# Performance work log

Hardware: AMD Instinct MI355X
Metric: run time of the kernel (lower is better)

Reference implementation:

```python
import jax, jax.numpy as jnp
import numpy as np

TWO_PI = 2.0 * np.pi
DAMP_VERTICAL = 1.0
DAMP_HORIZONTAL = 0.0


def _var(p, q, ra, rb, wvno, xka, xkb, dpth):
    # surf96 'var': layer eigenfunction products with evanescent-scaling (exp(-pex-sex))
    ra_s = jnp.where(ra > 0, ra, 1.0)
    rb_s = jnp.where(rb > 0, rb, 1.0)
    # P branch
    sinp_o = jnp.sin(p)
    fac_p = jnp.where(p < 16.0, jnp.exp(-2.0 * p), 0.0)
    cosp_e = (1.0 + fac_p) * 0.5
    sinp_e = (1.0 - fac_p) * 0.5
    lt_a = wvno < xka
    gt_a = wvno > xka
    pex = jnp.where(gt_a, p, 0.0)
    cosp = jnp.where(lt_a, jnp.cos(p), jnp.where(gt_a, cosp_e, 1.0))
    w = jnp.where(lt_a, sinp_o / ra_s, jnp.where(gt_a, sinp_e / ra_s, dpth))
    x = jnp.where(lt_a, -ra * sinp_o, jnp.where(gt_a, ra * sinp_e, 0.0))
    # S branch
    sinq_o = jnp.sin(q)
    fac_q = jnp.where(q < 16.0, jnp.exp(-2.0 * q), 0.0)
    cosq_e = (1.0 + fac_q) * 0.5
    sinq_e = (1.0 - fac_q) * 0.5
    lt_b = wvno < xkb
    gt_b = wvno > xkb
    sex = jnp.where(gt_b, q, 0.0)
    cosq = jnp.where(lt_b, jnp.cos(q), jnp.where(gt_b, cosq_e, 1.0))
    y = jnp.where(lt_b, sinq_o / rb_s, jnp.where(gt_b, sinq_e / rb_s, dpth))
    z = jnp.where(lt_b, -rb * sinq_o, jnp.where(gt_b, rb * sinq_e, 0.0))
    exa = pex + sex
    a0 = jnp.where(exa < 60.0, jnp.exp(-exa), 0.0)
    return (a0, cosp * cosq, cosp * y, cosp * z, cosq * w, cosq * x,
            x * y, x * z, w * y, w * z)


def _dnka(wvno2, gam, gammk, rho, a0, cpcq, cpy, cpz, cqw, cqx, xy, xz, wy, wz):
    # Dunkin's 5x5 compound matrix
    gamm1 = gam - 1.0
    twgm1 = gam + gamm1
    gmgmk = gam * gammk
    gmgm1 = gam * gamm1
    gm1sq = gamm1 * gamm1
    rho2 = rho * rho
    a0pq = a0 - cpcq
    t = -2.0 * wvno2
    c00 = cpcq - 2.0 * gmgm1 * a0pq - gmgmk * xz - wvno2 * gm1sq * wy
    c01 = (wvno2 * cpy - cqx) / rho
    c02 = -(twgm1 * a0pq + gammk * xz + wvno2 * gamm1 * wy) / rho
    c03 = (cpz - wvno2 * cqw) / rho
    c04 = -(2.0 * wvno2 * a0pq + xz + wvno2 * wvno2 * wy) / rho2
    c10 = (gmgmk * cpz - gm1sq * cqw) * rho
    c11 = cpcq
    c12 = gammk * cpz - gamm1 * cqw
    c13 = -wz
    c30 = (gm1sq * cpy - gmgmk * cqx) * rho
    c31 = -xy
    c32 = gamm1 * cpy - gammk * cqx
    c40 = -(2.0 * gmgmk * gm1sq * a0pq + gmgmk * gmgmk * xz + gm1sq * gm1sq * wy) * rho2
    c42 = -(gammk * gamm1 * twgm1 * a0pq + gam * gammk * gammk * xz + gamm1 * gm1sq * wy) * rho
    c20 = t * c42
    c21 = t * c32
    c22 = a0 + 2.0 * (cpcq - c00)
    c23 = t * c12
    c24 = t * c02
    rows = [[c00, c01, c02, c03, c04],
            [c10, c11, c12, c13, c03],
            [c20, c21, c22, c23, c24],
            [c30, c31, c32, c11, c01],
            [c40, c30, c42, c10, c00]]
    return jnp.stack([jnp.stack(r, axis=-1) for r in rows], axis=-2)


def _dltar4(wvno, omega, d, a, b, rho):
    # Rayleigh secular function, Dunkin algorithm, no water layer (llw=-1).
    # wvno/omega: (M, *extra) broadcast-compatible; d,a,b,rho: (M, L)
    extra = wvno.ndim - 1
    L = d.shape[-1]

    def lay(x):  # (M, L) -> (L, M, 1, ..., 1)
        return jnp.moveaxis(x, -1, 0).reshape((L, x.shape[0]) + (1,) * extra)

    dL, aL, bL, rhoL = lay(d), lay(a), lay(b), lay(rho)
    omega = jnp.maximum(omega, 1.0e-4)
    wvno2 = wvno * wvno

    # bottom half-space E vector
    xka = omega / aL[L - 1]
    xkb = omega / bL[L - 1]
    ra = jnp.sqrt(jnp.abs(wvno2 - xka * xka))
    rb = jnp.sqrt(jnp.abs(wvno2 - xkb * xkb))
    t = bL[L - 1] / omega
    gammk = 2.0 * t * t
    gam = gammk * wvno2
    gamm1 = gam - 1.0
    r = rhoL[L - 1]
    e = jnp.stack([r * r * (gamm1 * gamm1 - gam * gammk * ra * rb),
                   -r * ra,
                   r * (gamm1 - gammk * ra * rb),
                   r * rb,
                   wvno2 - ra * rb], axis=-1)

    xs = (dL[L - 2::-1], aL[L - 2::-1], bL[L - 2::-1], rhoL[L - 2::-1])

    def step(e, layer):
        dm, am, bm, rm = layer
        xka = omega / am
        xkb = omega / bm
        t = bm / omega
        gammk = 2.0 * t * t
        gam = gammk * wvno2
        ra = jnp.sqrt(jnp.abs(wvno2 - xka * xka))
        rb = jnp.sqrt(jnp.abs(wvno2 - xkb * xkb))
        p = ra * dm
        q = rb * dm
        vt = _var(p, q, ra, rb, wvno, xka, xkb, dm)
        ca = _dnka(wvno2, gam, gammk, rm, *vt)  # (..., 5, 5)
        ee = jnp.einsum('...j,...ji->...i', e, ca)
        t1 = jnp.max(jnp.abs(ee), axis=-1, keepdims=True)
        t1 = jnp.where(t1 < 1.0e-30, 1.0, t1)  # normc numerical-stability rescale
        return ee / t1, None

    e, _ = jax.lax.scan(step, e, xs)
    return e[..., 0]


def _forward(vlist, tlist, d, b, Clist):
    # Brocher empirical relations (initial_method == 'Brocher')
    a = 0.9409 + 2.0947 * b - 0.8206 * b**2 + 0.2683 * b**3 - 0.0251 * b**4
    rho = 1.6612 * a - 0.4721 * a**2 + 0.0671 * a**3 - 0.0043 * a**4 + 0.000106 * a**5

    omega = TWO_PI / tlist          # (M, P)
    wvno = omega / vlist
    e00 = _dltar4(wvno, omega, d, a, b, rho)  # (M, P)

    # normalization grid (torch.no_grad -> stop_gradient)
    omega_g = omega[:, None, :]                   # (M, 1, P)
    wvno_g = omega_g / Clist[None, :, None]       # (M, NC, P)
    det = jax.lax.stop_gradient(_dltar4(wvno_g, omega_g, d, a, b, rho))  # (M, NC, P)

    rng = jnp.max(det, axis=1) - jnp.min(det, axis=1)  # (M, P)
    e00 = e00 / rng
    e00 = jnp.power(0.1, jnp.abs(e00)) - 1.0           # compress_method == 'exp'
    e00_all = jnp.sum(jnp.abs(e00), axis=1) / e00.shape[-1]  # (M,)

    # vertical / horizontal damping regularization
    M, Lv = b.shape
    ev = jnp.eye(Lv, dtype=b.dtype)
    Lmat_v = 2.0 * ev - jnp.eye(Lv, k=1, dtype=b.dtype) - jnp.eye(Lv, k=-1, dtype=b.dtype)
    Lmat_v = Lmat_v.at[0, 0].set(1.0).at[Lv - 1, Lv - 1].set(1.0)
    eh = jnp.eye(M, dtype=b.dtype)
    Lmat_h = 2.0 * eh - jnp.eye(M, k=1, dtype=b.dtype) - jnp.eye(M, k=-1, dtype=b.dtype)
    Lmat_h = Lmat_h.at[0, 0].set(1.0).at[M - 1, M - 1].set(1.0)
    m_v = DAMP_VERTICAL * jnp.einsum('ij,mj->mi', Lmat_v, b) / Lv
    m_h = DAMP_HORIZONTAL * jnp.einsum('nm,ml->nl', Lmat_h, b) / Lv
    return e00_all + jnp.sum(jnp.abs(m_v), axis=1) + jnp.sum(jnp.abs(m_h), axis=1)


def setup_inputs() -> dict:
    key = jax.random.key(0)
    k1, k2, k3, k4 = jax.random.split(key, 4)
    M, L, P, NC = 64, 32, 100, 400
    tlist = jnp.sort(0.5 + 9.5 * jax.random.uniform(k1, (M, P), dtype=jnp.float32), axis=1)  # periods (s)
    vlist = 1.2 + 2.8 * jax.random.uniform(k2, (M, P), dtype=jnp.float32)                    # phase vel (km/s)
    d = 0.2 + 0.8 * jax.random.uniform(k3, (M, L), dtype=jnp.float32)                        # thickness (km)
    b = jnp.sort(1.5 + 3.0 * jax.random.uniform(k4, (M, L), dtype=jnp.float32), axis=1)      # Vs (km/s)
    Clist = jnp.linspace(1.0, 4.8, NC, dtype=jnp.float32)
    return {"vlist": vlist, "tlist": tlist, "d": d, "b": b, "Clist": Clist}


def reference(vlist, tlist, d, b, Clist):
    return _forward(vlist, tlist, d, b, Clist)
```

## Files before the change

### kernel.cpp

```cpp
#include <hip/hip_runtime.h>
#include <math.h>
#include <float.h>

#define Mdim 64
#define Ldim 32
#define Pdim 100
#define NCdim 400
#define EVALS_PER_P (NCdim + 1)
#define EVALS_PER_WAVE 128
#define WAVES_PER_M 314
#define BLOCKS_PER_M 79
#define NPTS (Mdim * Pdim)
#define WSLOT (Mdim * WAVES_PER_M)
#define TWO_PI_F 6.28318530717958647692f
#define INV_2PI_F 0.15915494309189535f
#define NLOG2E_F (-1.4426950408889634f)
#define LOG2_10TH (-3.3219280948873623f)

typedef float v2 __attribute__((ext_vector_type(2)));

__device__ __forceinline__ v2 mk2(float a, float b) { v2 r; r.x = a; r.y = b; return r; }
__device__ __forceinline__ v2 sel2(bool cx, bool cy, v2 a, v2 b) {
    return mk2(cx ? a.x : b.x, cy ? a.y : b.y);
}
__device__ __forceinline__ v2 sin2(v2 a) {
    return mk2(__builtin_amdgcn_sinf(a.x), __builtin_amdgcn_sinf(a.y));
}
__device__ __forceinline__ v2 cos2(v2 a) {
    return mk2(__builtin_amdgcn_cosf(a.x), __builtin_amdgcn_cosf(a.y));
}
__device__ __forceinline__ v2 exp22(v2 a) {
    return mk2(__builtin_amdgcn_exp2f(a.x), __builtin_amdgcn_exp2f(a.y));
}

struct alignas(16) LayerP {
    float inv_a2;
    float inv_b2;
    float b2two;
    float rm;
    float inv_rm;
    float rho2;
    float dm_i2p;
    float dm_nle;
};

template <bool RENORM>
__device__ __forceinline__ void layer_step(const LayerP& L,
                                           v2 wvno2, v2 wvno4, v2 tneg, v2 om2, v2 invom2,
                                           v2& e0, v2& e1, v2& e2, v2& e3, v2& e4)
{
    const v2 ra2 = wvno2 - om2 * L.inv_a2;
    const v2 rb2 = wvno2 - om2 * L.inv_b2;

    const v2 inv_ra = mk2(__builtin_amdgcn_rsqf(fabsf(ra2.x)),
                          __builtin_amdgcn_rsqf(fabsf(ra2.y)));
    const v2 inv_rb = mk2(__builtin_amdgcn_rsqf(fabsf(rb2.x)),
                          __builtin_amdgcn_rsqf(fabsf(rb2.y)));
    const v2 ra = mk2(fabsf(ra2.x), fabsf(ra2.y)) * inv_ra;
    const v2 rb = mk2(fabsf(rb2.x), fabsf(rb2.y)) * inv_rb;
    const v2 gammk = L.b2two * invom2;
    const v2 gam   = gammk * wvno2;

    const bool lt_ax = ra2.x < 0.0f, lt_ay = ra2.y < 0.0f;
    const bool lt_bx = rb2.x < 0.0f, lt_by = rb2.y < 0.0f;
    const v2 one = mk2(1.0f, 1.0f);

    v2 cosp, w, a0p;
    if (__all(!lt_ax && !lt_ay)) {
        const v2 pe    = ra * L.dm_nle;
        const v2 e_p   = exp22(pe);
        const v2 fac_p = e_p * e_p;
        cosp = 0.5f * fac_p + 0.5f;
        w    = (-0.5f * fac_p + 0.5f) * inv_ra;
        a0p  = e_p;
    } else if (__all(lt_ax && lt_ay)) {
        const v2 ppr = ra * L.dm_i2p;
        cosp = cos2(ppr);
        w    = sin2(ppr) * inv_ra;
        a0p  = one;
    } else {
        const v2 ppr   = ra * L.dm_i2p;
        const v2 pe    = ra * L.dm_nle;
        const v2 sp    = sin2(ppr);
        const v2 cp    = cos2(ppr);
        const v2 e_p   = exp22(pe);
        const v2 fac_p = e_p * e_p;
        cosp = sel2(lt_ax, lt_ay, cp, 0.5f * fac_p + 0.5f);
        w    = sel2(lt_ax, lt_ay, sp, -0.5f * fac_p + 0.5f) * inv_ra;
        a0p  = sel2(lt_ax, lt_ay, one, e_p);
    }

    v2 cosq, y, a0q;
    if (__all(!lt_bx && !lt_by)) {
        const v2 qe    = rb * L.dm_nle;
        const v2 e_q   = exp22(qe);
        const v2 fac_q = e_q * e_q;
        cosq = 0.5f * fac_q + 0.5f;
        y    = (-0.5f * fac_q + 0.5f) * inv_rb;
        a0q  = e_q;
    } else if (__all(lt_bx && lt_by)) {
        const v2 qqr = rb * L.dm_i2p;
        cosq = cos2(qqr);
        y    = sin2(qqr) * inv_rb;
        a0q  = one;
    } else {
        const v2 qqr   = rb * L.dm_i2p;
        const v2 qe    = rb * L.dm_nle;
        const v2 sq    = sin2(qqr);
        const v2 cq    = cos2(qqr);
        const v2 e_q   = exp22(qe);
        const v2 fac_q = e_q * e_q;
        cosq = sel2(lt_bx, lt_by, cq, 0.5f * fac_q + 0.5f);
        y    = sel2(lt_bx, lt_by, sq, -0.5f * fac_q + 0.5f) * inv_rb;
        a0q  = sel2(lt_bx, lt_by, one, e_q);
    }

    const v2 a0 = a0p * a0q;

    const v2 cpcq = cosp * cosq;
    const v2 cpy  = cosp * y;
    const v2 cqw  = cosq * w;
    const v2 wy   = w * y;
    const v2 cpz  = rb2 * cpy;
    const v2 cqx  = ra2 * cqw;
    const v2 wz   = rb2 * wy;
    const v2 xy   = ra2 * wy;
    const v2 xz   = ra2 * wz;

    const v2 gamm1 = gam - 1.0f;
    const v2 twgm1 = gam + gamm1;
    const v2 gmgmk = gam * gammk;
    const v2 gmgm1 = gam * gamm1;
    const v2 gm1sq = gamm1 * gamm1;
    const v2 a0pq  = a0 - cpcq;
    const float irho2 = L.inv_rm * L.inv_rm;

    const v2 c00 = cpcq - 2.0f * gmgm1 * a0pq - gmgmk * xz - wvno2 * gm1sq * wy;
    const v2 c01 = (wvno2 * cpy - cqx) * L.inv_rm;
    const v2 c02 = -(twgm1 * a0pq + gammk * xz + wvno2 * gamm1 * wy) * L.inv_rm;
    const v2 c03 = (cpz - wvno2 * cqw) * L.inv_rm;
    const v2 c04 = -(2.0f * wvno2 * a0pq + xz + wvno4 * wy) * irho2;
    const v2 c10 = (gmgmk * cpz - gm1sq * cqw) * L.rm;
    const v2 c11 = cpcq;
    const v2 c12 = gammk * cpz - gamm1 * cqw;
    const v2 c13 = -wz;
    const v2 c30 = (gm1sq * cpy - gmgmk * cqx) * L.rm;
    const v2 c31 = -xy;
    const v2 c32 = gamm1 * cpy - gammk * cqx;
    const v2 c40 = -(2.0f * gmgmk * gm1sq * a0pq + gmgmk * gmgmk * xz
                     + gm1sq * gm1sq * wy) * L.rho2;
    const v2 c42 = -(gammk * gamm1 * twgm1 * a0pq + gam * gammk * gammk * xz
                     + gamm1 * gm1sq * wy) * L.rm;
    const v2 c22 = a0 + 2.0f * (cpcq - c00);

    const v2 et2 = tneg * e2;

    const v2 ee0 = e0 * c00 + e1 * c10 + et2 * c42 + e3 * c30 + e4 * c40;
    const v2 ee1 = e0 * c01 + e1 * c11 + et2 * c32 + e3 * c31 + e4 * c30;
    const v2 ee2 = e0 * c02 + e1 * c12 + e2  * c22 + e3 * c32 + e4 * c42;
    const v2 ee3 = e0 * c03 + e1 * c13 + et2 * c12 + e3 * c11 + e4 * c10;
    const v2 ee4 = e0 * c04 + e1 * c03 + et2 * c02 + e3 * c01 + e4 * c00;

    if constexpr (RENORM) {
        float t1x = fmaxf(fmaxf(fabsf(ee0.x), fabsf(ee1.x)), fabsf(ee2.x));
        t1x = fmaxf(t1x, fmaxf(fabsf(ee3.x), fabsf(ee4.x)));
        float t1y = fmaxf(fmaxf(fabsf(ee0.y), fabsf(ee1.y)), fabsf(ee2.y));
        t1y = fmaxf(t1y, fmaxf(fabsf(ee3.y), fabsf(ee4.y)));
        t1x = fmaxf(t1x, 1e-30f);
        t1y = fmaxf(t1y, 1e-30f);
        const v2 inv = mk2(__builtin_amdgcn_rcpf(t1x), __builtin_amdgcn_rcpf(t1y));
        e0 = ee0 * inv;
        e1 = ee1 * inv;
        e2 = ee2 * inv;
        e3 = ee3 * inv;
        e4 = ee4 * inv;
    } else {
        e0 = ee0; e1 = ee1; e2 = ee2; e3 = ee3; e4 = ee4;
    }
}

__device__ __forceinline__ v2 dltar4_pk(v2 wvno2, v2 om2, v2 invom2,
                                        const LayerP* __restrict__ slay)
{
    const v2 wvno4 = wvno2 * wvno2;
    const v2 tneg  = -2.0f * wvno2;

    const LayerP H = slay[Ldim - 1];
    const v2 ra2h = wvno2 - om2 * H.inv_a2;
    const v2 rb2h = wvno2 - om2 * H.inv_b2;
    const v2 ra_h = mk2(__builtin_amdgcn_sqrtf(fabsf(ra2h.x)),
                        __builtin_amdgcn_sqrtf(fabsf(ra2h.y)));
    const v2 rb_h = mk2(__builtin_amdgcn_sqrtf(fabsf(rb2h.x)),
                        __builtin_amdgcn_sqrtf(fabsf(rb2h.y)));
    const v2 gammk_h = H.b2two * invom2;
    const v2 gam_h   = gammk_h * wvno2;
    const v2 gamm1_h = gam_h - 1.0f;
    const v2 rarb_h  = ra_h * rb_h;
    v2 e0 = H.rho2 * (gamm1_h * gamm1_h - gam_h * gammk_h * rarb_h);
    v2 e1 = -H.rm * ra_h;
    v2 e2 = H.rm * (gamm1_h - gammk_h * rarb_h);
    v2 e3 = H.rm * rb_h;
    v2 e4 = wvno2 - rarb_h;

    layer_step<true>(slay[Ldim - 2], wvno2, wvno4, tneg, om2, invom2,
                     e0, e1, e2, e3, e4);
    for (int l = Ldim - 3; l >= 1; l -= 2) {
        layer_step<false>(slay[l],     wvno2, wvno4, tneg, om2, invom2,
                          e0, e1, e2, e3, e4);
        layer_step<true> (slay[l - 1], wvno2, wvno4, tneg, om2, invom2,
                          e0, e1, e2, e3, e4);
    }
    return e0;
}

__global__ __launch_bounds__(256, 5)
void disp_kernel(const float* __restrict__ vlist, const float* __restrict__ tlist,
                 const float* __restrict__ dth,  const float* __restrict__ bvel,
                 const float* __restrict__ Clist,
                 float* __restrict__ pAmx, float* __restrict__ pAmn,
                 float* __restrict__ pBmx, float* __restrict__ pBmn,
                 float* __restrict__ e00f)
{
    __shared__ LayerP slay[Ldim];

    const int bid = blockIdx.x;
    const int m   = bid / BLOCKS_PER_M;
    const int wb  = bid - m * BLOCKS_PER_M;
    const int tid  = threadIdx.x;
    const int wid  = tid >> 6;
    const int lane = tid & 63;
    const int wv   = wb * 4 + wid;

    if (tid < Ldim) {
        const float bb = bvel[m * Ldim + tid];
        const float b2 = bb * bb;
        const float b3 = b2 * bb;
        const float b4 = b2 * b2;
        const float aa = 0.9409f + 2.0947f * bb - 0.8206f * b2
                         + 0.2683f * b3 - 0.0251f * b4;
        const float a2 = aa * aa;
        const float a3 = a2 * aa;
        const float a4 = a2 * a2;
        const float a5 = a4 * aa;
        const float rr = 1.6612f * aa - 0.4721f * a2 + 0.0671f * a3
                         - 0.0043f * a4 + 0.000106f * a5;
        const float dmv = dth[m * Ldim + tid];
        LayerP Lp;
        Lp.inv_a2 = 1.0f / (aa * aa);
        Lp.inv_b2 = 1.0f / (bb * bb);
        Lp.b2two  = 2.0f * bb * bb;
        Lp.rm     = rr;
        Lp.inv_rm = 1.0f / rr;
        Lp.rho2   = rr * rr;
        Lp.dm_i2p = dmv * INV_2PI_F;
        Lp.dm_nle = dmv * NLOG2E_F;
        slay[tid] = Lp;
    }
    __syncthreads();

    if (wv >= WAVES_PER_M) return;

    const int S  = wv * EVALS_PER_WAVE;
    const int p0 = S / EVALS_PER_P;
    const int c0 = S - p0 * EVALS_PER_P;

    int cx = c0 + lane;
    const bool crx = cx >= EVALS_PER_P;
    const int px = p0 + (crx ? 1 : 0);
    cx = crx ? cx - EVALS_PER_P : cx;
    const bool validx = px < Pdim;

    int cy = c0 + 64 + lane;
    const bool cry = cy >= EVALS_PER_P;
    const int py = p0 + (cry ? 1 : 0);
    cy = cry ? cy - EVALS_PER_P : cy;
    const bool validy = py < Pdim;

    const int mpx = m * Pdim + (validx ? px : 0);
    const int mpy = m * Pdim + (validy ? py : 0);
    const float omx = fmaxf(TWO_PI_F / tlist[mpx], 1.0e-4f);
    const float omy = fmaxf(TWO_PI_F / tlist[mpy], 1.0e-4f);
    const bool isCx = cx < NCdim;
    const bool isCy = cy < NCdim;
    const float denx = isCx ? Clist[cx] : vlist[mpx];
    const float deny = isCy ? Clist[cy] : vlist[mpy];
    const float wvx = omx * __builtin_amdgcn_rcpf(denx);
    const float wvy = omy * __builtin_amdgcn_rcpf(deny);

    const v2 om2    = mk2(omx * omx, omy * omy);
    const v2 invom2 = mk2(__builtin_amdgcn_rcpf(om2.x), __builtin_amdgcn_rcpf(om2.y));
    const v2 wvno2  = mk2(wvx * wvx, wvy * wvy);

    const v2 det = dltar4_pk(wvno2, om2, invom2, slay);

    if (validx && !isCx) e00f[m * Pdim + px] = det.x;
    if (validy && !isCy) e00f[m * Pdim + py] = det.y;

    const int pA = p0;
    const int pB = p0 + ((c0 + EVALS_PER_WAVE - 1) >= EVALS_PER_P ? 1 : 0);
    const int slot = m * WAVES_PER_M + wv;

    {
        const bool inAx = validx && isCx && (px == pA);
        const bool inAy = validy && isCy && (py == pA);
        float mxA = fmaxf(inAx ? det.x : -FLT_MAX, inAy ? det.y : -FLT_MAX);
        float mnA = fminf(inAx ? det.x :  FLT_MAX, inAy ? det.y :  FLT_MAX);
        for (int off = 32; off >= 1; off >>= 1) {
            mxA = fmaxf(mxA, __shfl_xor(mxA, off));
            mnA = fminf(mnA, __shfl_xor(mnA, off));
        }
        if (lane == 0) {
            pAmx[slot] = mxA;
            pAmn[slot] = mnA;
        }
    }
    if (pB != pA) {
        const bool inBx = validx && isCx && (px == pB);
        const bool inBy = validy && isCy && (py == pB);
        float mxB = fmaxf(inBx ? det.x : -FLT_MAX, inBy ? det.y : -FLT_MAX);
        float mnB = fminf(inBx ? det.x :  FLT_MAX, inBy ? det.y :  FLT_MAX);
        for (int off = 32; off >= 1; off >>= 1) {
            mxB = fmaxf(mxB, __shfl_xor(mxB, off));
            mnB = fminf(mnB, __shfl_xor(mnB, off));
        }
        if (lane == 0 && pB < Pdim) {
            pBmx[slot] = mxB;
            pBmn[slot] = mnB;
        }
    }
}

__global__ __launch_bounds__(64)
void epilogue_kernel(const float* __restrict__ pAmx, const float* __restrict__ pAmn,
                     const float* __restrict__ pBmx, const float* __restrict__ pBmn,
                     const float* __restrict__ e00f, const float* __restrict__ bvel,
                     float* __restrict__ out)
{
    const int m    = blockIdx.x;
    const int lane = threadIdx.x;

    float acc = 0.0f;
    for (int p = lane; p < Pdim; p += 64) {
        const int w0 = (EVALS_PER_P * p) / EVALS_PER_WAVE;
        const int w1 = (EVALS_PER_P * p + NCdim - 1) / EVALS_PER_WAVE;
        float mx = -FLT_MAX, mn = FLT_MAX;
        for (int w = w0; w <= w1; ++w) {
            const int s = m * WAVES_PER_M + w;
            const int pAw = (w * EVALS_PER_WAVE) / EVALS_PER_P;
            const float vmx = (pAw == p) ? pAmx[s] : pBmx[s];
            const float vmn = (pAw == p) ? pAmn[s] : pBmn[s];
            mx = fmaxf(mx, vmx);
            mn = fminf(mn, vmn);
        }
        const float en = e00f[m * Pdim + p] / (mx - mn);
        acc += 1.0f - __builtin_amdgcn_exp2f(fabsf(en) * LOG2_10TH);
    }

    float damp = 0.0f;
    if (lane < Ldim) {
        const float bb    = bvel[m * Ldim + lane];
        const float bprev = bvel[m * Ldim + ((lane == 0) ? 0 : lane - 1)];
        const float bnext = bvel[m * Ldim + ((lane == Ldim - 1) ? Ldim - 1 : lane + 1)];
        float tval;
        if (lane == 0)             tval = bb - bnext;
        else if (lane == Ldim - 1) tval = bb - bprev;
        else                       tval = 2.0f * bb - bprev - bnext;
        damp = fabsf(tval * (1.0f / (float)Ldim));
    }

    float tot = fmaf(acc, 1.0f / (float)Pdim, damp);
    for (int off = 32; off >= 1; off >>= 1)
        tot += __shfl_xor(tot, off);
    if (lane == 0) out[m] = tot;
}

extern "C" void kernel_launch(void* const* d_in, const int* in_sizes, int n_in,
                              void* d_out, int out_size, void* d_ws, size_t ws_size,
                              hipStream_t stream)
{
    const float* vlist = (const float*)d_in[0];
    const float* tlist = (const float*)d_in[1];
    const float* dth   = (const float*)d_in[2];
    const float* bvel  = (const float*)d_in[3];
    const float* Clist = (const float*)d_in[4];
    float* out = (float*)d_out;

    float* pAmx = (float*)d_ws;
    float* pAmn = pAmx + WSLOT;
    float* pBmx = pAmn + WSLOT;
    float* pBmn = pBmx + WSLOT;
    float* e00f = pBmn + WSLOT;

    hipLaunchKernelGGL(disp_kernel, dim3(Mdim * BLOCKS_PER_M), dim3(256), 0, stream,
                       vlist, tlist, dth, bvel, Clist, pAmx, pAmn, pBmx, pBmn, e00f);
    hipLaunchKernelGGL(epilogue_kernel, dim3(Mdim), dim3(64), 0, stream,
                       pAmx, pAmn, pBmx, pBmn, e00f, bvel, out);
}
```

Measured before the change: 256.0 us.

## Roll layer loop, drop all-oscillatory fast path, and factor Dunkin matrix terms

Replaces the unrolled pairs of templated layer steps with a single non-unrolled loop. A runtime renorm flag renormalises on every even layer. Removes the separate all-lanes-oscillatory branch, so that case now goes through the mixed path. Factors shared subexpressions in the compound-matrix coefficients to cut multiplies and live registers. The aim is smaller code and lower register pressure; the cost is a runtime branch per layer and extra exp work on wavefronts that are fully oscillatory.

```diff
diff --git a/kernel.cpp b/kernel.cpp
--- a/kernel.cpp
+++ b/kernel.cpp
@@ -44,9 +44,9 @@
     float dm_nle;
 };
 
-template <bool RENORM>
 __device__ __forceinline__ void layer_step(const LayerP& L,
-                                           v2 wvno2, v2 wvno4, v2 tneg, v2 om2, v2 invom2,
+                                           v2 wvno2, v2 tneg, v2 om2, v2 invom2,
+                                           bool renorm,
                                            v2& e0, v2& e1, v2& e2, v2& e3, v2& e4)
 {
     const v2 ra2 = wvno2 - om2 * L.inv_a2;
@@ -60,25 +60,18 @@
     const v2 rb = mk2(fabsf(rb2.x), fabsf(rb2.y)) * inv_rb;
     const v2 gammk = L.b2two * invom2;
     const v2 gam   = gammk * wvno2;
-
-    const bool lt_ax = ra2.x < 0.0f, lt_ay = ra2.y < 0.0f;
-    const bool lt_bx = rb2.x < 0.0f, lt_by = rb2.y < 0.0f;
-    const v2 one = mk2(1.0f, 1.0f);
+    const v2 one   = mk2(1.0f, 1.0f);
 
     v2 cosp, w, a0p;
-    if (__all(!lt_ax && !lt_ay)) {
+    if (__all(ra2.x >= 0.0f && ra2.y >= 0.0f)) {
         const v2 pe    = ra * L.dm_nle;
         const v2 e_p   = exp22(pe);
         const v2 fac_p = e_p * e_p;
         cosp = 0.5f * fac_p + 0.5f;
         w    = (-0.5f * fac_p + 0.5f) * inv_ra;
         a0p  = e_p;
-    } else if (__all(lt_ax && lt_ay)) {
-        const v2 ppr = ra * L.dm_i2p;
-        cosp = cos2(ppr);
-        w    = sin2(ppr) * inv_ra;
-        a0p  = one;
     } else {
+        const bool lt_ax = ra2.x < 0.0f, lt_ay = ra2.y < 0.0f;
         const v2 ppr   = ra * L.dm_i2p;
         const v2 pe    = ra * L.dm_nle;
         const v2 sp    = sin2(ppr);
@@ -91,19 +84,15 @@
     }
 
     v2 cosq, y, a0q;
-    if (__all(!lt_bx && !lt_by)) {
+    if (__all(rb2.x >= 0.0f && rb2.y >= 0.0f)) {
         const v2 qe    = rb * L.dm_nle;
         const v2 e_q   = exp22(qe);
         const v2 fac_q = e_q * e_q;
         cosq = 0.5f * fac_q + 0.5f;
         y    = (-0.5f * fac_q + 0.5f) * inv_rb;
         a0q  = e_q;
-    } else if (__all(lt_bx && lt_by)) {
-        const v2 qqr = rb * L.dm_i2p;
-        cosq = cos2(qqr);
-        y    = sin2(qqr) * inv_rb;
-        a0q  = one;
     } else {
+        const bool lt_bx = rb2.x < 0.0f, lt_by = rb2.y < 0.0f;
         const v2 qqr   = rb * L.dm_i2p;
         const v2 qe    = rb * L.dm_nle;
         const v2 sq    = sin2(qqr);
@@ -132,36 +121,39 @@
     const v2 gmgmk = gam * gammk;
     const v2 gmgm1 = gam * gamm1;
     const v2 gm1sq = gamm1 * gamm1;
-    const v2 a0pq  = a0 - cpcq;
+    const v2 A     = a0 - cpcq;
     const float irho2 = L.inv_rm * L.inv_rm;
 
-    const v2 c00 = cpcq - 2.0f * gmgm1 * a0pq - gmgmk * xz - wvno2 * gm1sq * wy;
+    const v2 gswy = gm1sq * wy;
+    const v2 w2wy = wvno2 * wy;
+    const v2 kxz  = gammk * xz;
+    const v2 gkxz = gam * kxz;
+
+    const v2 c00 = cpcq - 2.0f * (gmgm1 * A) - gkxz - wvno2 * gswy;
     const v2 c01 = (wvno2 * cpy - cqx) * L.inv_rm;
-    const v2 c02 = -(twgm1 * a0pq + gammk * xz + wvno2 * gamm1 * wy) * L.inv_rm;
+    const v2 c02 = -(twgm1 * A + kxz + gamm1 * w2wy) * L.inv_rm;
     const v2 c03 = (cpz - wvno2 * cqw) * L.inv_rm;
-    const v2 c04 = -(2.0f * wvno2 * a0pq + xz + wvno4 * wy) * irho2;
+    const v2 c04 = -(2.0f * (wvno2 * A) + xz + wvno2 * w2wy) * irho2;
     const v2 c10 = (gmgmk * cpz - gm1sq * cqw) * L.rm;
     const v2 c11 = cpcq;
     const v2 c12 = gammk * cpz - gamm1 * cqw;
-    const v2 c13 = -wz;
     const v2 c30 = (gm1sq * cpy - gmgmk * cqx) * L.rm;
-    const v2 c31 = -xy;
     const v2 c32 = gamm1 * cpy - gammk * cqx;
-    const v2 c40 = -(2.0f * gmgmk * gm1sq * a0pq + gmgmk * gmgmk * xz
-                     + gm1sq * gm1sq * wy) * L.rho2;
-    const v2 c42 = -(gammk * gamm1 * twgm1 * a0pq + gam * gammk * gammk * xz
-                     + gamm1 * gm1sq * wy) * L.rm;
+    const v2 gg  = gmgmk * gm1sq;
+    const v2 c40 = -(2.0f * (gg * A) + gmgmk * gkxz + gm1sq * gswy) * L.rho2;
+    const v2 g3  = gammk * gamm1;
+    const v2 c42 = -(g3 * twgm1 * A + gammk * gkxz + gamm1 * gswy) * L.rm;
     const v2 c22 = a0 + 2.0f * (cpcq - c00);
 
     const v2 et2 = tneg * e2;
 
     const v2 ee0 = e0 * c00 + e1 * c10 + et2 * c42 + e3 * c30 + e4 * c40;
-    const v2 ee1 = e0 * c01 + e1 * c11 + et2 * c32 + e3 * c31 + e4 * c30;
+    const v2 ee1 = e0 * c01 + e1 * c11 + et2 * c32 - e3 * xy + e4 * c30;
     const v2 ee2 = e0 * c02 + e1 * c12 + e2  * c22 + e3 * c32 + e4 * c42;
-    const v2 ee3 = e0 * c03 + e1 * c13 + et2 * c12 + e3 * c11 + e4 * c10;
+    const v2 ee3 = e0 * c03 - e1 * wz  + et2 * c12 + e3 * c11 + e4 * c10;
     const v2 ee4 = e0 * c04 + e1 * c03 + et2 * c02 + e3 * c01 + e4 * c00;
 
-    if constexpr (RENORM) {
+    if (renorm) {
         float t1x = fmaxf(fmaxf(fabsf(ee0.x), fabsf(ee1.x)), fabsf(ee2.x));
         t1x = fmaxf(t1x, fmaxf(fabsf(ee3.x), fabsf(ee4.x)));
         float t1y = fmaxf(fmaxf(fabsf(ee0.y), fabsf(ee1.y)), fabsf(ee2.y));
@@ -182,8 +174,7 @@
 __device__ __forceinline__ v2 dltar4_pk(v2 wvno2, v2 om2, v2 invom2,
                                         const LayerP* __restrict__ slay)
 {
-    const v2 wvno4 = wvno2 * wvno2;
-    const v2 tneg  = -2.0f * wvno2;
+    const v2 tneg = -2.0f * wvno2;
 
     const LayerP H = slay[Ldim - 1];
     const v2 ra2h = wvno2 - om2 * H.inv_a2;
@@ -202,13 +193,10 @@
     v2 e3 = H.rm * rb_h;
     v2 e4 = wvno2 - rarb_h;
 
-    layer_step<true>(slay[Ldim - 2], wvno2, wvno4, tneg, om2, invom2,
-                     e0, e1, e2, e3, e4);
-    for (int l = Ldim - 3; l >= 1; l -= 2) {
-        layer_step<false>(slay[l],     wvno2, wvno4, tneg, om2, invom2,
-                          e0, e1, e2, e3, e4);
-        layer_step<true> (slay[l - 1], wvno2, wvno4, tneg, om2, invom2,
-                          e0, e1, e2, e3, e4);
+#pragma clang loop unroll(disable)
+    for (int l = Ldim - 2; l >= 0; --l) {
+        layer_step(slay[l], wvno2, tneg, om2, invom2, (l & 1) == 0,
+                   e0, e1, e2, e3, e4);
     }
     return e0;
 }
```

After: 256.6 us. No clear change (+0.2%).
